# Optimization experiments

Hardware: AMD Instinct MI355X
Metric: run time of the kernel (lower is better)

## Reference

```python
import jax, jax.numpy as jnp
import numpy as np
from jax.experimental.ode import odeint

RN = 10000   # number of radial grid points (para['rn'])
RM = 200.0   # max radius (para['rm'])
NE = 1000    # number of eigenvalue samples (evl_tr)


def setup_inputs() -> dict:
    # Match the source driver exactly: evl = linspace(-0.05, 1, 1000),
    # r_dsc = linspace(rm/rn, rm, rn).
    evl = jnp.linspace(-0.05, 1.0, NE, dtype=jnp.float32)
    r_dsc = jnp.linspace(RM / RN, RM, RN, dtype=jnp.float32)
    return {"evl": evl, "r_dsc": r_dsc}


def reference(evl, r_dsc):
    E = evl.shape[0]
    # init state: rad = 0, rad' = 1  -> shape [E, 2]
    y0 = jnp.stack([jnp.zeros((E,), evl.dtype), jnp.ones((E,), evl.dtype)], axis=-1)

    def ode_func(y, t, evl):
        rad = y[:, 0]
        rad_d = y[:, 1]
        # ptl_rs = -2/r (Coulomb potential term), broadcast over eigenvalues
        rad_dd = (-2.0 / t - evl) * rad
        return jnp.stack([rad_d, rad_dd], axis=-1)

    # dopri5 adaptive RK45, same tolerances as torchdiffeq call.
    # Output: [RN, E, 2] solution sampled at every r_dsc point.
    return odeint(ode_func, y0, r_dsc, evl, rtol=1e-6, atol=1e-9)
```

## Files before the change

### kernel.cpp

```cpp
#include <hip/hip_runtime.h>

#define NE_  1000
#define RN_  10000
#define NI_  (RN_ - 1)

__device__ __forceinline__ float rcpf(float x) { return __builtin_amdgcn_rcpf(x); }

__device__ __forceinline__ void substeps_for(int p, int& S, float& invS) {
    if (p < 16)      { S = 4; invS = 0.25f; }
    else if (p < 64) { S = 2; invS = 0.5f;  }
    else             { S = 1; invS = 1.0f;  }
}

template <int NV>
__device__ __forceinline__ void rk4_step(float q1, float q2, float q3,
                                         float h2, float h, float h6,
                                         float a[NV], float b[NV]) {
#pragma unroll
    for (int v = 0; v < NV; ++v) {
        const float ya = a[v], yb = b[v];
        const float k1a = yb;              const float k1b = q1 * ya;
        const float y2a = fmaf(h2, k1a, ya); const float y2b = fmaf(h2, k1b, yb);
        const float k2a = y2b;             const float k2b = q2 * y2a;
        const float y3a = fmaf(h2, k2a, ya); const float y3b = fmaf(h2, k2b, yb);
        const float k3a = y3b;             const float k3b = q2 * y3a;
        const float y4a = fmaf(h,  k3a, ya); const float y4b = fmaf(h,  k3b, yb);
        const float k4a = y4b;             const float k4b = q3 * y4a;
        a[v] = fmaf(h6, fmaf(2.0f, k2a + k3a, k1a + k4a), ya);
        b[v] = fmaf(h6, fmaf(2.0f, k2b + k3b, k1b + k4b), yb);
    }
}

template <int NV>
__device__ __forceinline__ void advance_interval(float ta, float tb, float e,
                                                 int S, float invS,
                                                 float a[NV], float b[NV]) {
    const float hs = (tb - ta) * invS;
    const float h2 = 0.5f * hs;
    const float h6 = hs * (1.0f / 6.0f);
    for (int j = 0; j < S; ++j) {
        const float t0 = ta + hs * (float)j;
        const float q1 = fmaf(-2.0f, rcpf(t0),      -e);
        const float q2 = fmaf(-2.0f, rcpf(t0 + h2), -e);
        const float q3 = fmaf(-2.0f, rcpf(t0 + hs), -e);
        rk4_step<NV>(q1, q2, q3, h2, hs, h6, a, b);
    }
}

template <int CHUNK, int NV, bool STORE>
__device__ __forceinline__ void integrate_chunk(int p0, int p1, float step,
                                                float t0g, float e,
                                                float a[NV], float b[NV],
                                                float2* __restrict__ out, int ei) {
    if (p0 >= 64 && p0 + CHUNK == p1) {
        float tcur = fmaf((float)p0, step, t0g);
        float qcur = fmaf(-2.0f, rcpf(tcur), -e);
#pragma unroll
        for (int k = 0; k < CHUNK; ++k) {
            const float pf    = (float)(p0 + k);
            const float tmid  = fmaf(pf + 0.5f, step, t0g);
            const float tnext = fmaf(pf + 1.0f, step, t0g);
            const float h  = tnext - tcur;
            const float h2 = 0.5f * h;
            const float h6 = h * (1.0f / 6.0f);
            const float qmid  = fmaf(-2.0f, rcpf(tmid),  -e);
            const float qnext = fmaf(-2.0f, rcpf(tnext), -e);
            rk4_step<NV>(qcur, qmid, qnext, h2, h, h6, a, b);
            if (STORE) out[(size_t)(p0 + k + 1) * NE_ + ei] = make_float2(a[0], b[0]);
            tcur = tnext; qcur = qnext;
        }
    } else {
        for (int p = p0; p < p1; ++p) {
            const float ta = fmaf((float)p,       step, t0g);
            const float tb = fmaf((float)(p + 1), step, t0g);
            int S; float invS; substeps_for(p, S, invS);
            advance_interval<NV>(ta, tb, e, S, invS, a, b);
            if (STORE) out[(size_t)(p + 1) * NE_ + ei] = make_float2(a[0], b[0]);
        }
    }
}

template <int CHUNK>
__global__ void k_prop(const float* __restrict__ evl, const float* __restrict__ t,
                       float4* __restrict__ M, int nchunk) {
    const int tid = blockIdx.x * blockDim.x + threadIdx.x;
    if (tid >= NE_ * nchunk) return;
    const int ei = tid % NE_;
    const int c  = tid / NE_;
    const float e    = evl[ei];
    const float t0g  = t[0];
    const float step = (t[RN_ - 1] - t0g) * (1.0f / (float)NI_);
    const int p0 = c * CHUNK;
    const int p1 = min(p0 + CHUNK, NI_);
    float a[2] = {1.0f, 0.0f};
    float b[2] = {0.0f, 1.0f};
    integrate_chunk<CHUNK, 2, false>(p0, p1, step, t0g, e, a, b, nullptr, ei);
    M[tid] = make_float4(a[0], b[0], a[1], b[1]);
}

__device__ __forceinline__ float4 mmul(float4 B, float4 A) {
    float4 r;
    r.x = B.x * A.x + B.z * A.y;
    r.y = B.y * A.x + B.w * A.y;
    r.z = B.x * A.z + B.z * A.w;
    r.w = B.y * A.z + B.w * A.w;
    return r;
}

template <int KPL>
__global__ void k_scan_wave(const float4* __restrict__ M, float2* __restrict__ Yst,
                            int nchunk) {
    const int gid  = blockIdx.x * blockDim.x + threadIdx.x;
    const int wid  = gid >> 6;
    const int lane = gid & 63;
    if (wid >= NE_) return;
    const int ei = wid;
    const int c0 = lane * KPL;

    float4 Mloc[KPL];
#pragma unroll
    for (int k = 0; k < KPL; ++k) {
        const int c = c0 + k;
        Mloc[k] = (c < nchunk) ? M[(size_t)c * NE_ + ei]
                               : make_float4(1.f, 0.f, 0.f, 1.f);
    }
    float4 C = make_float4(1.f, 0.f, 0.f, 1.f);
#pragma unroll
    for (int k = 0; k < KPL; ++k) C = mmul(Mloc[k], C);

    for (int off = 1; off < 64; off <<= 1) {
        float4 o;
        o.x = __shfl_up(C.x, off);
        o.y = __shfl_up(C.y, off);
        o.z = __shfl_up(C.z, off);
        o.w = __shfl_up(C.w, off);
        if (lane >= off) C = mmul(C, o);
    }
    float4 P;
    P.x = __shfl_up(C.x, 1);
    P.y = __shfl_up(C.y, 1);
    P.z = __shfl_up(C.z, 1);
    P.w = __shfl_up(C.w, 1);
    if (lane == 0) P = make_float4(1.f, 0.f, 0.f, 1.f);

    float ya = P.z, yb = P.w;
#pragma unroll
    for (int k = 0; k < KPL; ++k) {
        const int c = c0 + k;
        if (c < nchunk) {
            Yst[(size_t)c * NE_ + ei] = make_float2(ya, yb);
            const float4 m = Mloc[k];
            const float na = m.x * ya + m.z * yb;
            const float nb = m.y * ya + m.w * yb;
            ya = na; yb = nb;
        }
    }
}

template <int CHUNK>
__global__ void k_out(const float* __restrict__ evl, const float* __restrict__ t,
                      const float2* __restrict__ Yst, float2* __restrict__ out,
                      int nchunk) {
    const int tid = blockIdx.x * blockDim.x + threadIdx.x;
    if (tid >= NE_ * nchunk) return;
    const int ei = tid % NE_;
    const int c  = tid / NE_;
    const float e    = evl[ei];
    const float t0g  = t[0];
    const float step = (t[RN_ - 1] - t0g) * (1.0f / (float)NI_);
    const int p0 = c * CHUNK;
    const int p1 = min(p0 + CHUNK, NI_);
    const float2 y0 = Yst[tid];
    float a[1] = {y0.x};
    float b[1] = {y0.y};
    if (c == 0) out[ei] = make_float2(0.0f, 1.0f);
    integrate_chunk<CHUNK, 1, true>(p0, p1, step, t0g, e, a, b, out, ei);
}

__global__ void k_serial(const float* __restrict__ evl, const float* __restrict__ t,
                         float2* __restrict__ out) {
    const int ei = blockIdx.x * blockDim.x + threadIdx.x;
    if (ei >= NE_) return;
    const float e    = evl[ei];
    const float t0g  = t[0];
    const float step = (t[RN_ - 1] - t0g) * (1.0f / (float)NI_);
    float a[1] = {0.0f};
    float b[1] = {1.0f};
    out[ei] = make_float2(0.0f, 1.0f);
    for (int p = 0; p < NI_; ++p) {
        const float ta = fmaf((float)p,       step, t0g);
        const float tb = fmaf((float)(p + 1), step, t0g);
        int S; float invS; substeps_for(p, S, invS);
        advance_interval<1>(ta, tb, e, S, invS, a, b);
        out[(size_t)(p + 1) * NE_ + ei] = make_float2(a[0], b[0]);
    }
}

extern "C" void kernel_launch(void* const* d_in, const int* in_sizes, int n_in,
                              void* d_out, int out_size, void* d_ws, size_t ws_size,
                              hipStream_t stream) {
    const float* evl = (const float*)d_in[0];
    const float* t   = (const float*)d_in[1];
    float2* out = (float2*)d_out;

    auto need = [](int nch) {
        return (size_t)NE_ * nch * (sizeof(float4) + sizeof(float2));
    };

    int nchunk;
    if      (ws_size >= need(1000)) nchunk = 1000;
    else if (ws_size >= need(500))  nchunk = 500;
    else if (ws_size >= need(200))  nchunk = 200;
    else {
        k_serial<<<(NE_ + 255) / 256, 256, 0, stream>>>(evl, t, out);
        return;
    }

    float4* M   = (float4*)d_ws;
    float2* Yst = (float2*)((char*)d_ws + (size_t)NE_ * nchunk * sizeof(float4));
    const int ntask  = NE_ * nchunk;
    const int blocks = (ntask + 255) / 256;

    if (nchunk == 1000) {
        k_prop<10><<<blocks, 256, 0, stream>>>(evl, t, M, nchunk);
        k_scan_wave<16><<<250, 256, 0, stream>>>(M, Yst, nchunk);
        k_out<10><<<blocks, 256, 0, stream>>>(evl, t, Yst, out, nchunk);
    } else if (nchunk == 500) {
        k_prop<20><<<blocks, 256, 0, stream>>>(evl, t, M, nchunk);
        k_scan_wave<8><<<250, 256, 0, stream>>>(M, Yst, nchunk);
        k_out<20><<<blocks, 256, 0, stream>>>(evl, t, Yst, out, nchunk);
    } else {
        k_prop<50><<<blocks, 256, 0, stream>>>(evl, t, M, nchunk);
        k_scan_wave<4><<<250, 256, 0, stream>>>(M, Yst, nchunk);
        k_out<50><<<blocks, 256, 0, stream>>>(evl, t, Yst, out, nchunk);
    }
}
```

Measured before the change: 127.3 us.

## Replace wave-parallel matrix scan with per-eigenvalue sequential scan, use 500 chunks

Swaps the 64-lane shuffle-based prefix scan over 2x2 transfer matrices for a simple serial scan with one thread per eigenvalue, batching 25 matrix loads at a time. The default chunk count drops from 1000 to 500, doubling the interval length per thread in the propagate and output kernels. The aim is to remove the shuffle and matrix-product overhead of the parallel scan. In exchange, the scan runs on only 1000 threads with a long dependent chain, which risks being latency-bound.

```diff
diff --git a/kernel.cpp b/kernel.cpp
--- a/kernel.cpp
+++ b/kernel.cpp
@@ -19,13 +19,13 @@
 #pragma unroll
     for (int v = 0; v < NV; ++v) {
         const float ya = a[v], yb = b[v];
-        const float k1a = yb;              const float k1b = q1 * ya;
+        const float k1a = yb;                const float k1b = q1 * ya;
         const float y2a = fmaf(h2, k1a, ya); const float y2b = fmaf(h2, k1b, yb);
-        const float k2a = y2b;             const float k2b = q2 * y2a;
+        const float k2a = y2b;               const float k2b = q2 * y2a;
         const float y3a = fmaf(h2, k2a, ya); const float y3b = fmaf(h2, k2b, yb);
-        const float k3a = y3b;             const float k3b = q2 * y3a;
+        const float k3a = y3b;               const float k3b = q2 * y3a;
         const float y4a = fmaf(h,  k3a, ya); const float y4b = fmaf(h,  k3b, yb);
-        const float k4a = y4b;             const float k4b = q3 * y4a;
+        const float k4a = y4b;               const float k4b = q3 * y4a;
         a[v] = fmaf(h6, fmaf(2.0f, k2a + k3a, k1a + k4a), ya);
         b[v] = fmaf(h6, fmaf(2.0f, k2b + k3b, k1b + k4b), yb);
     }
@@ -98,60 +98,22 @@
     M[tid] = make_float4(a[0], b[0], a[1], b[1]);
 }
 
-__device__ __forceinline__ float4 mmul(float4 B, float4 A) {
-    float4 r;
-    r.x = B.x * A.x + B.z * A.y;
-    r.y = B.y * A.x + B.w * A.y;
-    r.z = B.x * A.z + B.z * A.w;
-    r.w = B.y * A.z + B.w * A.w;
-    return r;
-}
-
-template <int KPL>
-__global__ void k_scan_wave(const float4* __restrict__ M, float2* __restrict__ Yst,
-                            int nchunk) {
-    const int gid  = blockIdx.x * blockDim.x + threadIdx.x;
-    const int wid  = gid >> 6;
-    const int lane = gid & 63;
-    if (wid >= NE_) return;
-    const int ei = wid;
-    const int c0 = lane * KPL;
-
-    float4 Mloc[KPL];
+template <int BATCH>
+__global__ void k_scan_lin(const float4* __restrict__ M, float2* __restrict__ Yst,
+                           int nchunk) {
+    const int ei = blockIdx.x * blockDim.x + threadIdx.x;
+    if (ei >= NE_) return;
+    float ya = 0.0f, yb = 1.0f;
+    for (int c0 = 0; c0 < nchunk; c0 += BATCH) {
+        float4 m[BATCH];
 #pragma unroll
-    for (int k = 0; k < KPL; ++k) {
-        const int c = c0 + k;
-        Mloc[k] = (c < nchunk) ? M[(size_t)c * NE_ + ei]
-                               : make_float4(1.f, 0.f, 0.f, 1.f);
-    }
-    float4 C = make_float4(1.f, 0.f, 0.f, 1.f);
+        for (int k = 0; k < BATCH; ++k)
+            m[k] = M[(size_t)(c0 + k) * NE_ + ei];
 #pragma unroll
-    for (int k = 0; k < KPL; ++k) C = mmul(Mloc[k], C);
-
-    for (int off = 1; off < 64; off <<= 1) {
-        float4 o;
-        o.x = __shfl_up(C.x, off);
-        o.y = __shfl_up(C.y, off);
-        o.z = __shfl_up(C.z, off);
-        o.w = __shfl_up(C.w, off);
-        if (lane >= off) C = mmul(C, o);
-    }
-    float4 P;
-    P.x = __shfl_up(C.x, 1);
-    P.y = __shfl_up(C.y, 1);
-    P.z = __shfl_up(C.z, 1);
-    P.w = __shfl_up(C.w, 1);
-    if (lane == 0) P = make_float4(1.f, 0.f, 0.f, 1.f);
-
-    float ya = P.z, yb = P.w;
-#pragma unroll
-    for (int k = 0; k < KPL; ++k) {
-        const int c = c0 + k;
-        if (c < nchunk) {
-            Yst[(size_t)c * NE_ + ei] = make_float2(ya, yb);
-            const float4 m = Mloc[k];
-            const float na = m.x * ya + m.z * yb;
-            const float nb = m.y * ya + m.w * yb;
+        for (int k = 0; k < BATCH; ++k) {
+            Yst[(size_t)(c0 + k) * NE_ + ei] = make_float2(ya, yb);
+            const float na = fmaf(m[k].x, ya, m[k].z * yb);
+            const float nb = fmaf(m[k].y, ya, m[k].w * yb);
             ya = na; yb = nb;
         }
     }
@@ -208,9 +170,8 @@
     };
 
     int nchunk;
-    if      (ws_size >= need(1000)) nchunk = 1000;
-    else if (ws_size >= need(500))  nchunk = 500;
-    else if (ws_size >= need(200))  nchunk = 200;
+    if      (ws_size >= need(500)) nchunk = 500;
+    else if (ws_size >= need(200)) nchunk = 200;
     else {
         k_serial<<<(NE_ + 255) / 256, 256, 0, stream>>>(evl, t, out);
         return;
@@ -221,17 +182,13 @@
     const int ntask  = NE_ * nchunk;
     const int blocks = (ntask + 255) / 256;
 
-    if (nchunk == 1000) {
-        k_prop<10><<<blocks, 256, 0, stream>>>(evl, t, M, nchunk);
-        k_scan_wave<16><<<250, 256, 0, stream>>>(M, Yst, nchunk);
-        k_out<10><<<blocks, 256, 0, stream>>>(evl, t, Yst, out, nchunk);
-    } else if (nchunk == 500) {
+    if (nchunk == 500) {
         k_prop<20><<<blocks, 256, 0, stream>>>(evl, t, M, nchunk);
-        k_scan_wave<8><<<250, 256, 0, stream>>>(M, Yst, nchunk);
+        k_scan_lin<25><<<4, 256, 0, stream>>>(M, Yst, nchunk);
         k_out<20><<<blocks, 256, 0, stream>>>(evl, t, Yst, out, nchunk);
     } else {
         k_prop<50><<<blocks, 256, 0, stream>>>(evl, t, M, nchunk);
-        k_scan_wave<4><<<250, 256, 0, stream>>>(M, Yst, nchunk);
+        k_scan_lin<25><<<4, 256, 0, stream>>>(M, Yst, nchunk);
         k_out<50><<<blocks, 256, 0, stream>>>(evl, t, Yst, out, nchunk);
     }
 }
```

New measurement: 150.8 us. +18.5%, slower.
